# Performance work log

Hardware: AMD Instinct MI355X
Metric: run time of the kernel (lower is better)

Reference implementation:

```python
import jax, jax.numpy as jnp
import numpy as np

EPS = 1e-5

def _layernorm(x, w, b):
    mu = jnp.mean(x, axis=-1, keepdims=True)
    var = jnp.mean(jnp.square(x - mu), axis=-1, keepdims=True)
    return (x - mu) * jax.lax.rsqrt(var + EPS) * w + b

def setup_inputs() -> dict:
    key = jax.random.key(0)
    ks = jax.random.split(key, 6)
    B, Np, Nc, D, P = 2, 512, 512, 128, 128
    p_embed = jax.random.normal(ks[0], (B, Np, D), dtype=jnp.float32)
    c_embed = jax.random.normal(ks[1], (B, Nc, D), dtype=jnp.float32)
    p_mask = jnp.ones((B, Np), dtype=bool)
    c_mask = jnp.ones((B, Nc), dtype=bool)
    ln_p_w = jnp.ones((D,), jnp.float32)
    ln_p_b = jnp.zeros((D,), jnp.float32)
    ln_c_w = jnp.ones((D,), jnp.float32)
    ln_c_b = jnp.zeros((D,), jnp.float32)
    W_out = jax.random.normal(ks[2], (P, D), dtype=jnp.float32) / np.sqrt(D)
    b_out = jax.random.normal(ks[3], (P,), dtype=jnp.float32) * 0.01
    return {"p_embed": p_embed, "c_embed": c_embed, "p_mask": p_mask,
            "c_mask": c_mask, "ln_p_w": ln_p_w, "ln_p_b": ln_p_b,
            "ln_c_w": ln_c_w, "ln_c_b": ln_c_b, "W_out": W_out, "b_out": b_out}

def reference(p_embed, c_embed, p_mask, c_mask, ln_p_w, ln_p_b, ln_c_w, ln_c_b, W_out, b_out):
    # inter_mask[b,i,j] = p_mask[b,i] & c_mask[b,j]
    inter_mask = p_mask[..., :, None] & c_mask[..., None, :]
    p = _layernorm(p_embed, ln_p_w, ln_p_b)  # [B,Np,D]
    c = _layernorm(c_embed, ln_c_w, ln_c_b)  # [B,Nc,D]
    # einsum '...ik,...jk->...ijk' followed by Linear(D->P), fused into one
    # contraction so the [B,Np,Nc,D] intermediate is never materialized:
    # out[b,i,j,h] = sum_k p[b,i,k]*c[b,j,k]*W_out[h,k] + b_out[h]
    inter = jnp.einsum('bik,bjk,hk->bijh', p, c, W_out) + b_out
    inter = inter * inter_mask[..., None].astype(inter.dtype)
    return inter, inter_mask
```

## Files before the change

### kernel.cpp

```cpp
#include <hip/hip_runtime.h>
#include <hip/hip_bf16.h>

#define BATCH 2
#define NP 512
#define NC 512
#define DD 128
#define PP 128

typedef __bf16 bf16_t;
typedef __bf16 bf16x8 __attribute__((ext_vector_type(8)));
typedef __bf16 bf16x2 __attribute__((ext_vector_type(2)));
typedef float f32x4 __attribute__((ext_vector_type(4)));

__global__ __launch_bounds__(64) void ln_kernel(
    const float* __restrict__ p, const float* __restrict__ c,
    const float* __restrict__ pw, const float* __restrict__ pb,
    const float* __restrict__ cw, const float* __restrict__ cb,
    float* __restrict__ p_ln, bf16_t* __restrict__ c_bf) {
    int row = blockIdx.x;
    bool isP = row < BATCH * NP;
    int crow = row - BATCH * NP;
    const float* x  = isP ? p + (size_t)row * DD : c + (size_t)crow * DD;
    const float* w  = isP ? pw : cw;
    const float* bs = isP ? pb : cb;
    int t = threadIdx.x;
    float2 v = *(const float2*)&x[2 * t];
    float s  = v.x + v.y;
    float sq = v.x * v.x + v.y * v.y;
    for (int o = 32; o; o >>= 1) {
        s  += __shfl_xor(s, o);
        sq += __shfl_xor(sq, o);
    }
    float mu  = s * (1.0f / 128.0f);
    float var = sq * (1.0f / 128.0f) - mu * mu;
    float rs  = rsqrtf(var + 1e-5f);
    float2 wv = *(const float2*)&w[2 * t];
    float2 bv = *(const float2*)&bs[2 * t];
    float o0 = (v.x - mu) * rs * wv.x + bv.x;
    float o1 = (v.y - mu) * rs * wv.y + bv.y;
    if (isP) {
        float2 o2; o2.x = o0; o2.y = o1;
        *(float2*)&p_ln[(size_t)row * DD + 2 * t] = o2;
    } else {
        bf16x2 o2; o2[0] = (bf16_t)o0; o2[1] = (bf16_t)o1;
        *(bf16x2*)&c_bf[(size_t)crow * DD + 2 * t] = o2;
    }
}

__global__ __launch_bounds__(256, 4) void inter_kernel(
    const float* __restrict__ p_ln, const bf16_t* __restrict__ c_bf,
    const float* __restrict__ W, const float* __restrict__ b_out,
    const int* __restrict__ p_mask,
    const int* __restrict__ c_mask,
    float* __restrict__ out) {
    __shared__ bf16_t As[128][136];

    int blk = blockIdx.x;
    int jq = blk & 3;
    int i  = (blk >> 2) & (NP - 1);
    int b  = blk >> 11;
    int j0 = jq * 128;

    int t = threadIdx.x;
    int lane = t & 63;
    int wave = t >> 6;
    int l16 = lane & 15, q = lane >> 4;

    const bf16_t* cbb = c_bf + ((size_t)(b * NC + j0)) * DD;
    {
        int col = (t & 15) * 8;
        int rg = t >> 4;
        #pragma unroll
        for (int pass = 0; pass < 8; ++pass) {
            int r = pass * 16 + rg;
            *(bf16x8*)&As[r][col] = *(const bf16x8*)&cbb[(size_t)r * DD + col];
        }
    }

    int pm = p_mask[b * NP + i];
    const int* cmb = c_mask + b * NC + j0;
    float sc[8];
    #pragma unroll
    for (int jt = 0; jt < 8; ++jt)
        sc[jt] = (pm != 0 && cmb[jt * 16 + l16] != 0) ? 1.0f : 0.0f;

    const float* pr = p_ln + ((size_t)(b * NP + i)) * DD;
    bf16x8 wf[2][4];
    #pragma unroll
    for (int ht = 0; ht < 2; ++ht) {
        int h = wave * 32 + ht * 16 + l16;
        const float* wr = W + (size_t)h * DD;
        #pragma unroll
        for (int kt = 0; kt < 4; ++kt) {
            int k = kt * 32 + q * 8;
            float4 w0 = *(const float4*)&wr[k];
            float4 w1 = *(const float4*)&wr[k + 4];
            float4 pv0 = *(const float4*)&pr[k];
            float4 pv1 = *(const float4*)&pr[k + 4];
            bf16x8 f;
            f[0] = (bf16_t)(w0.x * pv0.x); f[1] = (bf16_t)(w0.y * pv0.y);
            f[2] = (bf16_t)(w0.z * pv0.z); f[3] = (bf16_t)(w0.w * pv0.w);
            f[4] = (bf16_t)(w1.x * pv1.x); f[5] = (bf16_t)(w1.y * pv1.y);
            f[6] = (bf16_t)(w1.z * pv1.z); f[7] = (bf16_t)(w1.w * pv1.w);
            wf[ht][kt] = f;
        }
    }

    f32x4 bias0 = *(const f32x4*)&b_out[wave * 32 + q * 4];
    f32x4 bias1 = *(const f32x4*)&b_out[wave * 32 + 16 + q * 4];

    int cc   = lane & 7;
    int idxA = ((((cc & 3) << 4) | (lane >> 3))) << 2;
    int idxB = idxA + 32;

    __syncthreads();

    size_t outbase = (((size_t)b * NP + i) * NC + j0) * PP;
    #pragma unroll 2
    for (int jt = 0; jt < 8; ++jt) {
        int jr = jt * 16 + l16;
        bf16x8 cf[4];
        #pragma unroll
        for (int kt = 0; kt < 4; ++kt)
            cf[kt] = *(const bf16x8*)&As[jr][kt * 32 + q * 8];
        f32x4 acc0 = {0.f, 0.f, 0.f, 0.f};
        f32x4 acc1 = {0.f, 0.f, 0.f, 0.f};
        #pragma unroll
        for (int kt = 0; kt < 4; ++kt) {
            acc0 = __builtin_amdgcn_mfma_f32_16x16x32_bf16(wf[0][kt], cf[kt], acc0, 0, 0, 0);
            acc1 = __builtin_amdgcn_mfma_f32_16x16x32_bf16(wf[1][kt], cf[kt], acc1, 0, 0, 0);
        }
        f32x4 a0 = (acc0 + bias0) * sc[jt];
        f32x4 a1 = (acc1 + bias1) * sc[jt];

        f32x4 vA, vB;
        #pragma unroll
        for (int r = 0; r < 4; ++r) {
            int s0A = __builtin_amdgcn_ds_bpermute(idxA, __float_as_int(a0[r]));
            int s1A = __builtin_amdgcn_ds_bpermute(idxA, __float_as_int(a1[r]));
            vA[r] = __int_as_float(cc < 4 ? s0A : s1A);
            int s0B = __builtin_amdgcn_ds_bpermute(idxB, __float_as_int(a0[r]));
            int s1B = __builtin_amdgcn_ds_bpermute(idxB, __float_as_int(a1[r]));
            vB[r] = __int_as_float(cc < 4 ? s0B : s1B);
        }
        int rowA = jt * 16 + (lane >> 3);
        int rowB = rowA + 8;
        *(f32x4*)(out + outbase + (size_t)rowA * PP + wave * 32 + cc * 4) = vA;
        *(f32x4*)(out + outbase + (size_t)rowB * PP + wave * 32 + cc * 4) = vB;
    }

    if (t < 128) {
        size_t mbase = (size_t)BATCH * NP * NC * PP;
        out[mbase + ((size_t)b * NP + i) * NC + j0 + t] =
            (pm != 0 && cmb[t] != 0) ? 1.0f : 0.0f;
    }
}

extern "C" void kernel_launch(void* const* d_in, const int* in_sizes, int n_in,
                              void* d_out, int out_size, void* d_ws, size_t ws_size,
                              hipStream_t stream) {
    const float* p_embed = (const float*)d_in[0];
    const float* c_embed = (const float*)d_in[1];
    const int* p_mask = (const int*)d_in[2];
    const int* c_mask = (const int*)d_in[3];
    const float* ln_p_w = (const float*)d_in[4];
    const float* ln_p_b = (const float*)d_in[5];
    const float* ln_c_w = (const float*)d_in[6];
    const float* ln_c_b = (const float*)d_in[7];
    const float* W_out  = (const float*)d_in[8];
    const float* b_out  = (const float*)d_in[9];
    float* out = (float*)d_out;

    float* p_ln = (float*)d_ws;
    bf16_t* c_bf = (bf16_t*)(p_ln + (size_t)BATCH * NP * DD);

    ln_kernel<<<BATCH * (NP + NC), 64, 0, stream>>>(
        p_embed, c_embed, ln_p_w, ln_p_b, ln_c_w, ln_c_b, p_ln, c_bf);
    inter_kernel<<<BATCH * NP * (NC / 128), 256, 0, stream>>>(
        p_ln, c_bf, W_out, b_out, p_mask, c_mask, out);
}
```

Before: 293.4 us.

## Process eight p-rows per block to reuse the shared C tile and W

Each block now handles a tile of 8 consecutive i-rows instead of one. It loads the bf16 C tile, the W rows and the 8 p rows once, then loops over the rows, forming W*p fragments from shared memory. This amortizes the shared-memory fill and global loads across more output, at the cost of a grid eight times smaller and a reduced occupancy hint.

Result: faster. 284.4 us (-3.1%).

```diff
diff --git a/kernel.cpp b/kernel.cpp
--- a/kernel.cpp
+++ b/kernel.cpp
@@ -6,6 +6,7 @@
 #define NC 512
 #define DD 128
 #define PP 128
+#define ITILE 8
 
 typedef __bf16 bf16_t;
 typedef __bf16 bf16x8 __attribute__((ext_vector_type(8)));
@@ -47,18 +48,20 @@
     }
 }
 
-__global__ __launch_bounds__(256, 4) void inter_kernel(
+__global__ __launch_bounds__(256, 2) void inter_kernel(
     const float* __restrict__ p_ln, const bf16_t* __restrict__ c_bf,
     const float* __restrict__ W, const float* __restrict__ b_out,
     const int* __restrict__ p_mask,
     const int* __restrict__ c_mask,
     float* __restrict__ out) {
-    __shared__ bf16_t As[128][136];
+    __shared__ bf16_t Cs[128][136];
+    __shared__ float  Ps[ITILE][DD];
 
     int blk = blockIdx.x;
     int jq = blk & 3;
-    int i  = (blk >> 2) & (NP - 1);
-    int b  = blk >> 11;
+    int it = (blk >> 2) & 63;
+    int b  = blk >> 8;
+    int i0 = it * ITILE;
     int j0 = jq * 128;
 
     int t = threadIdx.x;
@@ -73,86 +76,115 @@
         #pragma unroll
         for (int pass = 0; pass < 8; ++pass) {
             int r = pass * 16 + rg;
-            *(bf16x8*)&As[r][col] = *(const bf16x8*)&cbb[(size_t)r * DD + col];
-        }
-    }
-
-    int pm = p_mask[b * NP + i];
+            *(bf16x8*)&Cs[r][col] = *(const bf16x8*)&cbb[(size_t)r * DD + col];
+        }
+    }
+    {
+        int pr_ = t >> 5;
+        int pc  = (t & 31) * 4;
+        *(f32x4*)&Ps[pr_][pc] =
+            *(const f32x4*)&p_ln[((size_t)(b * NP + i0 + pr_)) * DD + pc];
+    }
+
+    f32x4 wreg[2][4][2];
+    #pragma unroll
+    for (int ht = 0; ht < 2; ++ht) {
+        const float* wr = W + (size_t)(wave * 32 + ht * 16 + l16) * DD;
+        #pragma unroll
+        for (int kt = 0; kt < 4; ++kt) {
+            int k = kt * 32 + q * 8;
+            wreg[ht][kt][0] = *(const f32x4*)&wr[k];
+            wreg[ht][kt][1] = *(const f32x4*)&wr[k + 4];
+        }
+    }
+
+    int pmv[ITILE];
+    #pragma unroll
+    for (int ii = 0; ii < ITILE; ++ii)
+        pmv[ii] = p_mask[b * NP + i0 + ii];
     const int* cmb = c_mask + b * NC + j0;
     float sc[8];
     #pragma unroll
     for (int jt = 0; jt < 8; ++jt)
-        sc[jt] = (pm != 0 && cmb[jt * 16 + l16] != 0) ? 1.0f : 0.0f;
-
-    const float* pr = p_ln + ((size_t)(b * NP + i)) * DD;
-    bf16x8 wf[2][4];
-    #pragma unroll
-    for (int ht = 0; ht < 2; ++ht) {
-        int h = wave * 32 + ht * 16 + l16;
-        const float* wr = W + (size_t)h * DD;
+        sc[jt] = (cmb[jt * 16 + l16] != 0) ? 1.0f : 0.0f;
+    int4 cm4 = *(const int4*)&cmb[(t & 31) * 4];
+
+    f32x4 bias0 = *(const f32x4*)&b_out[wave * 32 + q * 4];
+    f32x4 bias1 = *(const f32x4*)&b_out[wave * 32 + 16 + q * 4];
+
+    int cc   = lane & 7;
+    int idxA = ((((cc & 3) << 4) | (lane >> 3))) << 2;
+    int idxB = idxA + 32;
+
+    __syncthreads();
+
+    {
+        int mr = t >> 5;
+        int mc = (t & 31) * 4;
+        size_t mbase = (size_t)BATCH * NP * NC * PP;
+        f32x4 mv;
+        mv[0] = (pmv[mr] != 0 && cm4.x != 0) ? 1.0f : 0.0f;
+        mv[1] = (pmv[mr] != 0 && cm4.y != 0) ? 1.0f : 0.0f;
+        mv[2] = (pmv[mr] != 0 && cm4.z != 0) ? 1.0f : 0.0f;
+        mv[3] = (pmv[mr] != 0 && cm4.w != 0) ? 1.0f : 0.0f;
+        *(f32x4*)&out[mbase + ((size_t)b * NP + i0 + mr) * NC + j0 + mc] = mv;
+    }
+
+    #pragma unroll 1
+    for (int ii = 0; ii < ITILE; ++ii) {
+        bf16x8 wf[2][4];
         #pragma unroll
         for (int kt = 0; kt < 4; ++kt) {
             int k = kt * 32 + q * 8;
-            float4 w0 = *(const float4*)&wr[k];
-            float4 w1 = *(const float4*)&wr[k + 4];
-            float4 pv0 = *(const float4*)&pr[k];
-            float4 pv1 = *(const float4*)&pr[k + 4];
-            bf16x8 f;
-            f[0] = (bf16_t)(w0.x * pv0.x); f[1] = (bf16_t)(w0.y * pv0.y);
-            f[2] = (bf16_t)(w0.z * pv0.z); f[3] = (bf16_t)(w0.w * pv0.w);
-            f[4] = (bf16_t)(w1.x * pv1.x); f[5] = (bf16_t)(w1.y * pv1.y);
-            f[6] = (bf16_t)(w1.z * pv1.z); f[7] = (bf16_t)(w1.w * pv1.w);
-            wf[ht][kt] = f;
-        }
-    }
-
-    f32x4 bias0 = *(const f32x4*)&b_out[wave * 32 + q * 4];
-    f32x4 bias1 = *(const f32x4*)&b_out[wave * 32 + 16 + q * 4];
-
-    int cc   = lane & 7;
-    int idxA = ((((cc & 3) << 4) | (lane >> 3))) << 2;
-    int idxB = idxA + 32;
-
-    __syncthreads();
-
-    size_t outbase = (((size_t)b * NP + i) * NC + j0) * PP;
-    #pragma unroll 2
-    for (int jt = 0; jt < 8; ++jt) {
-        int jr = jt * 16 + l16;
-        bf16x8 cf[4];
-        #pragma unroll
-        for (int kt = 0; kt < 4; ++kt)
-            cf[kt] = *(const bf16x8*)&As[jr][kt * 32 + q * 8];
-        f32x4 acc0 = {0.f, 0.f, 0.f, 0.f};
-        f32x4 acc1 = {0.f, 0.f, 0.f, 0.f};
-        #pragma unroll
-        for (int kt = 0; kt < 4; ++kt) {
-            acc0 = __builtin_amdgcn_mfma_f32_16x16x32_bf16(wf[0][kt], cf[kt], acc0, 0, 0, 0);
-            acc1 = __builtin_amdgcn_mfma_f32_16x16x32_bf16(wf[1][kt], cf[kt], acc1, 0, 0, 0);
-        }
-        f32x4 a0 = (acc0 + bias0) * sc[jt];
-        f32x4 a1 = (acc1 + bias1) * sc[jt];
-
-        f32x4 vA, vB;
-        #pragma unroll
-        for (int r = 0; r < 4; ++r) {
-            int s0A = __builtin_amdgcn_ds_bpermute(idxA, __float_as_int(a0[r]));
-            int s1A = __builtin_amdgcn_ds_bpermute(idxA, __float_as_int(a1[r]));
-            vA[r] = __int_as_float(cc < 4 ? s0A : s1A);
-            int s0B = __builtin_amdgcn_ds_bpermute(idxB, __float_as_int(a0[r]));
-            int s1B = __builtin_amdgcn_ds_bpermute(idxB, __float_as_int(a1[r]));
-            vB[r] = __int_as_float(cc < 4 ? s0B : s1B);
-        }
-        int rowA = jt * 16 + (lane >> 3);
-        int rowB = rowA + 8;
-        *(f32x4*)(out + outbase + (size_t)rowA * PP + wave * 32 + cc * 4) = vA;
-        *(f32x4*)(out + outbase + (size_t)rowB * PP + wave * 32 + cc * 4) = vB;
-    }
-
-    if (t < 128) {
-        size_t mbase = (size_t)BATCH * NP * NC * PP;
-        out[mbase + ((size_t)b * NP + i) * NC + j0 + t] =
-            (pm != 0 && cmb[t] != 0) ? 1.0f : 0.0f;
+            f32x4 pv0 = *(const f32x4*)&Ps[ii][k];
+            f32x4 pv1 = *(const f32x4*)&Ps[ii][k + 4];
+            #pragma unroll
+            for (int ht = 0; ht < 2; ++ht) {
+                f32x4 w0 = wreg[ht][kt][0];
+                f32x4 w1 = wreg[ht][kt][1];
+                bf16x8 f;
+                f[0] = (bf16_t)(w0[0] * pv0[0]); f[1] = (bf16_t)(w0[1] * pv0[1]);
+                f[2] = (bf16_t)(w0[2] * pv0[2]); f[3] = (bf16_t)(w0[3] * pv0[3]);
+                f[4] = (bf16_t)(w1[0] * pv1[0]); f[5] = (bf16_t)(w1[1] * pv1[1]);
+                f[6] = (bf16_t)(w1[2] * pv1[2]); f[7] = (bf16_t)(w1[3] * pv1[3]);
+                wf[ht][kt] = f;
+            }
+        }
+        float pmf = (pmv[ii] != 0) ? 1.0f : 0.0f;
+        size_t outbase = (((size_t)b * NP + i0 + ii) * NC + j0) * PP;
+        #pragma unroll 2
+        for (int jt = 0; jt < 8; ++jt) {
+            int jr = jt * 16 + l16;
+            bf16x8 cf[4];
+            #pragma unroll
+            for (int kt = 0; kt < 4; ++kt)
+                cf[kt] = *(const bf16x8*)&Cs[jr][kt * 32 + q * 8];
+            f32x4 acc0 = {0.f, 0.f, 0.f, 0.f};
+            f32x4 acc1 = {0.f, 0.f, 0.f, 0.f};
+            #pragma unroll
+            for (int kt = 0; kt < 4; ++kt) {
+                acc0 = __builtin_amdgcn_mfma_f32_16x16x32_bf16(wf[0][kt], cf[kt], acc0, 0, 0, 0);
+                acc1 = __builtin_amdgcn_mfma_f32_16x16x32_bf16(wf[1][kt], cf[kt], acc1, 0, 0, 0);
+            }
+            float s = sc[jt] * pmf;
+            f32x4 a0 = (acc0 + bias0) * s;
+            f32x4 a1 = (acc1 + bias1) * s;
+
+            f32x4 vA, vB;
+            #pragma unroll
+            for (int r = 0; r < 4; ++r) {
+                int s0A = __builtin_amdgcn_ds_bpermute(idxA, __float_as_int(a0[r]));
+                int s1A = __builtin_amdgcn_ds_bpermute(idxA, __float_as_int(a1[r]));
+                vA[r] = __int_as_float(cc < 4 ? s0A : s1A);
+                int s0B = __builtin_amdgcn_ds_bpermute(idxB, __float_as_int(a0[r]));
+                int s1B = __builtin_amdgcn_ds_bpermute(idxB, __float_as_int(a1[r]));
+                vB[r] = __int_as_float(cc < 4 ? s0B : s1B);
+            }
+            int rowA = jt * 16 + (lane >> 3);
+            int rowB = rowA + 8;
+            *(f32x4*)(out + outbase + (size_t)rowA * PP + wave * 32 + cc * 4) = vA;
+            *(f32x4*)(out + outbase + (size_t)rowB * PP + wave * 32 + cc * 4) = vB;
+        }
     }
 }
 
@@ -176,6 +208,6 @@
 
     ln_kernel<<<BATCH * (NP + NC), 64, 0, stream>>>(
         p_embed, c_embed, ln_p_w, ln_p_b, ln_c_w, ln_c_b, p_ln, c_bf);
-    inter_kernel<<<BATCH * NP * (NC / 128), 256, 0, stream>>>(
+    inter_kernel<<<BATCH * (NP / ITILE) * (NC / 128), 256, 0, stream>>>(
         p_ln, c_bf, W_out, b_out, p_mask, c_mask, out);
 }
```
